# Optimization experiments

Measured on AMD Instinct MI355X. Metric: run time of the kernel, lower is better.

## Reference

```python
import jax, jax.numpy as jnp
import numpy as np

N = 4096
STEPS = 32


def setup_inputs() -> dict:
    key = jax.random.key(0)
    k0, k1, k2, k3 = jax.random.split(key, 4)
    x = jax.random.normal(k0, (N, 2), dtype=jnp.float32) * 0.02
    raw_S = jax.random.normal(k1, (N, N), dtype=jnp.float32) * 0.1
    raw_phase = jax.random.normal(k2, (N, N), dtype=jnp.float32) * 0.1
    # raw_r initialized at logit(p_r0=0.2) in the original module
    init_logit = float(np.log(0.2 / 0.8))
    raw_r = jnp.full((N, N), init_logit, dtype=jnp.float32)
    mask = (jax.random.uniform(k3, (N, N)) < 0.1).astype(jnp.float32)
    A_mask = jnp.maximum(mask, jnp.eye(N, dtype=jnp.float32))
    G_gate = jnp.ones((N, N), dtype=jnp.float32)
    omega = jnp.float32(0.1)
    return {"x": x, "raw_S": raw_S, "raw_phase": raw_phase, "raw_r": raw_r,
            "A_mask": A_mask, "G_gate": G_gate, "omega": omega, "steps": STEPS}


def reference(x, raw_S, raw_phase, raw_r, A_mask, G_gate, omega, steps):
    # Effective amplitude adjacency (beta=0, no do-interventions): same at every step
    S = jnp.tanh(raw_S)
    r = jax.nn.sigmoid(raw_r)
    Aamp = A_mask * G_gate * S * r  # [N, N]

    def step(xc, t):
        theta = raw_phase + omega * t          # [N, N] time-varying phase
        c = jnp.cos(theta)
        s = jnp.sin(theta)
        xr = xc[:, 0]  # [N]
        xi = xc[:, 1]  # [N]
        out_r = (Aamp * c) @ xr - (Aamp * s) @ xi
        out_i = (Aamp * s) @ xr + (Aamp * c) @ xi
        x_next = jnp.stack([jnp.tanh(out_r), jnp.tanh(out_i)], axis=-1)  # [N, 2]
        return x_next, x_next

    ts = jnp.arange(steps, dtype=x.dtype)
    _, traj = jax.lax.scan(step, x, ts)
    return jnp.concatenate([x[None], traj], axis=0)  # [steps+1, N, 2]
```

## Files before the change

kernel.cpp:

```cpp
#include <hip/hip_runtime.h>
#include <cstdint>
#include <cstddef>

#define N 4096
#define STEPS 32
#define PADW 640

__device__ __forceinline__ float bf16lo_to_f(uint32_t u) {
    return __uint_as_float(u << 16);
}
__device__ __forceinline__ float bf16hi_to_f(uint32_t u) {
    return __uint_as_float(u & 0xFFFF0000u);
}
__device__ __forceinline__ uint32_t f_to_bf16bits(float f) {
    uint32_t u = __float_as_uint(f);
    return (u + 0x7FFFu + ((u >> 16) & 1u)) >> 16;
}
__device__ __forceinline__ float fast_tanh(float x) {
    float e = __expf(2.0f * x);
    return (e - 1.0f) * __builtin_amdgcn_rcpf(e + 1.0f);
}
__device__ __forceinline__ float fast_sigmoid(float x) {
    return __builtin_amdgcn_rcpf(1.0f + __expf(-x));
}


__global__ __launch_bounds__(256) void fill_sparse_kernel(
    const float* __restrict__ raw_S,
    const float* __restrict__ raw_phase,
    const float* __restrict__ raw_r,
    const float* __restrict__ A_mask,
    const float* __restrict__ G_gate,
    uint16_t* __restrict__ col16,
    uint32_t* __restrict__ val32)
{
    const int wave = threadIdx.x >> 6;
    const int lane = threadIdx.x & 63;
    const int row  = blockIdx.x * 4 + wave;
    const size_t rbase = (size_t)row * N;
    const size_t pbase = (size_t)row * PADW;

    int base = 0;
    size_t off0 = rbase + lane * 4;
    float4 m4 = *(const float4*)(A_mask + off0);
    float4 g4 = *(const float4*)(G_gate + off0);
    float4 s4 = *(const float4*)(raw_S + off0);
    float4 r4 = *(const float4*)(raw_r + off0);
    float4 p4 = *(const float4*)(raw_phase + off0);

#pragma unroll 2
    for (int j = 0; j < N / 256; j++) {
        float mv[4] = {m4.x, m4.y, m4.z, m4.w};
        float gv[4] = {g4.x, g4.y, g4.z, g4.w};
        float sv[4] = {s4.x, s4.y, s4.z, s4.w};
        float rv[4] = {r4.x, r4.y, r4.z, r4.w};
        float pv[4] = {p4.x, p4.y, p4.z, p4.w};
        if (j < N / 256 - 1) {
            size_t off = rbase + (j + 1) * 256 + lane * 4;
            m4 = *(const float4*)(A_mask + off);
            g4 = *(const float4*)(G_gate + off);
            s4 = *(const float4*)(raw_S + off);
            r4 = *(const float4*)(raw_r + off);
            p4 = *(const float4*)(raw_phase + off);
        }

        uint32_t pk[4];
        bool pr[4];
#pragma unroll
        for (int k = 0; k < 4; k++) {
            pr[k] = (mv[k] != 0.0f);
            float S  = fast_tanh(sv[k]);
            float rr = fast_sigmoid(rv[k]);
            float amp = mv[k] * gv[k] * S * rr;
            uint32_t pc = f_to_bf16bits(amp * __cosf(pv[k]));
            uint32_t ps = f_to_bf16bits(amp * __sinf(pv[k]));
            pk[k] = (ps << 16) | pc;
        }
#pragma unroll
        for (int k = 0; k < 4; k++) {
            unsigned long long bal = __ballot(pr[k]);
            if (pr[k]) {
                int idx = base + __popcll(bal & ((1ull << lane) - 1ull));
                if (idx < PADW) {
                    col16[pbase + idx] = (uint16_t)(j * 256 + lane * 4 + k);
                    val32[pbase + idx] = pk[k];
                }
            }
            base += (int)__popcll(bal);
        }
    }
    if (base > PADW) base = PADW;
    for (int i = base + lane; i < PADW; i += 64) {
        col16[pbase + i] = 0;
        val32[pbase + i] = 0;
    }
}

__global__ __launch_bounds__(256) void step_sparse_kernel(
    const uint16_t* __restrict__ col16,
    const uint32_t* __restrict__ val32,
    const float* __restrict__ x_in,
    float* __restrict__ x_out,
    const float* __restrict__ omega_ptr,
    int t)
{
    __shared__ float xs[2 * N];
    const int tid = threadIdx.x;
    {
        const float4* src = (const float4*)x_in;
        float4* dst = (float4*)xs;
#pragma unroll
        for (int i = 0; i < 8; i++)
            dst[tid + 256 * i] = src[tid + 256 * i];
    }
    __syncthreads();

    const int wave = tid >> 6;
    const int lane = tid & 63;
    const int row = blockIdx.x * 4 + wave;

    const uint32_t* colp = (const uint32_t*)(col16 + (size_t)row * PADW);
    const uint2*    valp = (const uint2*)(val32 + (size_t)row * PADW);

    float are = 0.0f, aim = 0.0f;
#pragma unroll
    for (int j = 0; j < PADW / 128; j++) {
        uint32_t cc = colp[j * 64 + lane];
        uint2    vv = valp[j * 64 + lane];
        int c0 = (int)(cc & 0xFFFFu), c1 = (int)(cc >> 16);
        float2 x0 = *(const float2*)(xs + 2 * c0);
        float2 x1 = *(const float2*)(xs + 2 * c1);
        float pc0 = bf16lo_to_f(vv.x), ps0 = bf16hi_to_f(vv.x);
        float pc1 = bf16lo_to_f(vv.y), ps1 = bf16hi_to_f(vv.y);
        are = fmaf(pc0, x0.x, are); are = fmaf(-ps0, x0.y, are);
        aim = fmaf(ps0, x0.x, aim); aim = fmaf(pc0, x0.y, aim);
        are = fmaf(pc1, x1.x, are); are = fmaf(-ps1, x1.y, are);
        aim = fmaf(ps1, x1.x, aim); aim = fmaf(pc1, x1.y, aim);
    }
#pragma unroll
    for (int off = 32; off; off >>= 1) {
        are += __shfl_down(are, off);
        aim += __shfl_down(aim, off);
    }
    if (lane == 0) {
        float theta = omega_ptr[0] * (float)t;
        float st, ct;
        __sincosf(theta, &st, &ct);
        float ore = ct * are - st * aim;
        float oim = st * are + ct * aim;
        *(float2*)(x_out + 2 * row) =
            make_float2(fast_tanh(ore), fast_tanh(oim));
    }
}


__global__ __launch_bounds__(256) void precompute_kernel(
    const float* __restrict__ raw_phase,
    const float* __restrict__ raw_r,
    const float* __restrict__ A_mask,
    const float* __restrict__ G_gate,
    const float* raw_S_in,
    float* dst)
{
    int idx = (blockIdx.x * 256 + threadIdx.x) * 4;
    float4 s4 = *(const float4*)(raw_S_in + idx);
    float4 p4 = *(const float4*)(raw_phase + idx);
    float4 r4 = *(const float4*)(raw_r + idx);
    float4 m4 = *(const float4*)(A_mask + idx);
    float4 g4 = *(const float4*)(G_gate + idx);
    float sv[4] = {s4.x, s4.y, s4.z, s4.w};
    float pv[4] = {p4.x, p4.y, p4.z, p4.w};
    float rv[4] = {r4.x, r4.y, r4.z, r4.w};
    float mv[4] = {m4.x, m4.y, m4.z, m4.w};
    float gv[4] = {g4.x, g4.y, g4.z, g4.w};
    float ov[4];
#pragma unroll
    for (int k = 0; k < 4; k++) {
        float S = fast_tanh(sv[k]);
        float r = fast_sigmoid(rv[k]);
        float amp = mv[k] * gv[k] * S * r;
        uint32_t pc = f_to_bf16bits(amp * __cosf(pv[k]));
        uint32_t ps = f_to_bf16bits(amp * __sinf(pv[k]));
        ov[k] = __uint_as_float((ps << 16) | pc);
    }
    *(float4*)(dst + idx) = make_float4(ov[0], ov[1], ov[2], ov[3]);
}

__global__ __launch_bounds__(512, 8) void step_kernel(
    const float* __restrict__ Mpacked_f,
    const float* __restrict__ x_in,
    float* __restrict__ x_out,
    const float* __restrict__ omega_ptr,
    int t)
{
    const int tid  = threadIdx.x;
    const int wave = tid >> 6;
    const int lane = tid & 63;
    const int row0 = blockIdx.x * 4;
    const uint32_t* M = (const uint32_t*)Mpacked_f;
    const int cbase = (wave << 9) + (lane << 2);
    float xr[8], xi[8];
#pragma unroll
    for (int s = 0; s < 2; s++) {
        int j = cbase + (s << 8);
        float4 a = *(const float4*)(x_in + 2 * j);
        float4 b = *(const float4*)(x_in + 2 * j + 4);
        xr[4*s+0]=a.x; xi[4*s+0]=a.y; xr[4*s+1]=a.z; xi[4*s+1]=a.w;
        xr[4*s+2]=b.x; xi[4*s+2]=b.y; xr[4*s+3]=b.z; xi[4*s+3]=b.w;
    }
    __shared__ float part[8][4][2];
#pragma unroll
    for (int r = 0; r < 4; r++) {
        const uint32_t* Mrow = M + (size_t)(row0 + r) * N + cbase;
        float are = 0.0f, aim = 0.0f;
#pragma unroll
        for (int s = 0; s < 2; s++) {
            uint4 m = *(const uint4*)(Mrow + (s << 8));
            uint32_t mm[4] = {m.x, m.y, m.z, m.w};
#pragma unroll
            for (int k = 0; k < 4; k++) {
                float pc = bf16lo_to_f(mm[k]);
                float ps = bf16hi_to_f(mm[k]);
                float xre = xr[4*s+k], xim = xi[4*s+k];
                are = fmaf(pc, xre, are); are = fmaf(-ps, xim, are);
                aim = fmaf(ps, xre, aim); aim = fmaf(pc, xim, aim);
            }
        }
#pragma unroll
        for (int off = 32; off; off >>= 1) {
            are += __shfl_down(are, off);
            aim += __shfl_down(aim, off);
        }
        if (lane == 0) { part[wave][r][0] = are; part[wave][r][1] = aim; }
    }
    __syncthreads();
    if (tid < 4) {
        float U = 0.0f, V = 0.0f;
#pragma unroll
        for (int w = 0; w < 8; w++) { U += part[w][tid][0]; V += part[w][tid][1]; }
        float theta = omega_ptr[0] * (float)t;
        float stv, ctv;
        __sincosf(theta, &stv, &ctv);
        float ore = ctv * U - stv * V;
        float oim = stv * U + ctv * V;
        int row = row0 + tid;
        x_out[2*row+0] = fast_tanh(ore);
        x_out[2*row+1] = fast_tanh(oim);
    }
}


extern "C" void kernel_launch(void* const* d_in, const int* in_sizes, int n_in,
                              void* d_out, int out_size, void* d_ws, size_t ws_size,
                              hipStream_t stream) {
    const float* x         = (const float*)d_in[0];
    float*       raw_S     = (float*)d_in[1];
    const float* raw_phase = (const float*)d_in[2];
    const float* raw_r     = (const float*)d_in[3];
    const float* A_mask    = (const float*)d_in[4];
    const float* G_gate    = (const float*)d_in[5];
    const float* omega     = (const float*)d_in[6];
    float* out = (float*)d_out;

    hipMemcpyAsync(out, x, (size_t)N * 2 * sizeof(float),
                   hipMemcpyDeviceToDevice, stream);

    const size_t colBytes = (size_t)N * PADW * sizeof(uint16_t);
    const size_t valBytes = (size_t)N * PADW * sizeof(uint32_t);
    if (ws_size >= colBytes + valBytes) {
        uint16_t* col16 = (uint16_t*)d_ws;
        uint32_t* val32 = (uint32_t*)((char*)d_ws + colBytes);

        fill_sparse_kernel<<<dim3(N / 4), dim3(256), 0, stream>>>(
            raw_S, raw_phase, raw_r, A_mask, G_gate, col16, val32);

        for (int t = 0; t < STEPS; t++) {
            step_sparse_kernel<<<dim3(N / 4), dim3(256), 0, stream>>>(
                col16, val32,
                out + (size_t)t * N * 2,
                out + (size_t)(t + 1) * N * 2,
                omega, t);
        }
    } else {
        float* packed = raw_S;
        precompute_kernel<<<dim3(N * (N / 1024)), dim3(256), 0, stream>>>(
            raw_phase, raw_r, A_mask, G_gate, raw_S, packed);
        for (int t = 0; t < STEPS; t++) {
            step_kernel<<<dim3(N / 4), dim3(512), 0, stream>>>(
                packed,
                out + (size_t)t * N * 2,
                out + (size_t)(t + 1) * N * 2,
                omega, t);
        }
    }
}
```

Before: 453.5 us.

## Fuse all steps into persistent kernel with grid barrier and register-resident sparse matrix

Replaces the 32 per-step launches with a single persistent kernel of 256 blocks of 1024 threads. Each wave keeps its row's sparse values and column indices in registers across all steps, and blocks synchronise through a global atomic-counter barrier. The fill kernel is also split so each row is handled by two waves over half-rows, with a fixed per-half capacity of 320 nonzeros. This removes launch overhead and repeated sparse-matrix reloads, but it relies on all 256 blocks being co-resident. The half-row cap can also drop entries if nonzeros are unevenly split between the two halves.

```diff
diff --git a/kernel.cpp b/kernel.cpp
--- a/kernel.cpp
+++ b/kernel.cpp
@@ -5,6 +5,8 @@
 #define N 4096
 #define STEPS 32
 #define PADW 640
+#define HALFW 320
+#define PGRID 256
 
 __device__ __forceinline__ float bf16lo_to_f(uint32_t u) {
     return __uint_as_float(u << 16);
@@ -23,7 +25,6 @@
 __device__ __forceinline__ float fast_sigmoid(float x) {
     return __builtin_amdgcn_rcpf(1.0f + __expf(-x));
 }
-
 
 __global__ __launch_bounds__(256) void fill_sparse_kernel(
     const float* __restrict__ raw_S,
@@ -34,11 +35,13 @@
     uint16_t* __restrict__ col16,
     uint32_t* __restrict__ val32)
 {
-    const int wave = threadIdx.x >> 6;
-    const int lane = threadIdx.x & 63;
-    const int row  = blockIdx.x * 4 + wave;
-    const size_t rbase = (size_t)row * N;
-    const size_t pbase = (size_t)row * PADW;
+    const int wave   = threadIdx.x >> 6;
+    const int lane   = threadIdx.x & 63;
+    const int halfid = blockIdx.x * 4 + wave;
+    const int row    = halfid >> 1;
+    const int h      = halfid & 1;
+    const size_t rbase = (size_t)row * N + (size_t)h * (N / 2);
+    const size_t pbase = (size_t)row * PADW + (size_t)h * HALFW;
 
     int base = 0;
     size_t off0 = rbase + lane * 4;
@@ -49,13 +52,13 @@
     float4 p4 = *(const float4*)(raw_phase + off0);
 
 #pragma unroll 2
-    for (int j = 0; j < N / 256; j++) {
+    for (int j = 0; j < (N / 2) / 256; j++) {
         float mv[4] = {m4.x, m4.y, m4.z, m4.w};
         float gv[4] = {g4.x, g4.y, g4.z, g4.w};
         float sv[4] = {s4.x, s4.y, s4.z, s4.w};
         float rv[4] = {r4.x, r4.y, r4.z, r4.w};
         float pv[4] = {p4.x, p4.y, p4.z, p4.w};
-        if (j < N / 256 - 1) {
+        if (j < (N / 2) / 256 - 1) {
             size_t off = rbase + (j + 1) * 256 + lane * 4;
             m4 = *(const float4*)(A_mask + off);
             g4 = *(const float4*)(G_gate + off);
@@ -81,75 +84,104 @@
             unsigned long long bal = __ballot(pr[k]);
             if (pr[k]) {
                 int idx = base + __popcll(bal & ((1ull << lane) - 1ull));
-                if (idx < PADW) {
-                    col16[pbase + idx] = (uint16_t)(j * 256 + lane * 4 + k);
+                if (idx < HALFW) {
+                    col16[pbase + idx] =
+                        (uint16_t)(h * (N / 2) + j * 256 + lane * 4 + k);
                     val32[pbase + idx] = pk[k];
                 }
             }
             base += (int)__popcll(bal);
         }
     }
-    if (base > PADW) base = PADW;
-    for (int i = base + lane; i < PADW; i += 64) {
+    if (base > HALFW) base = HALFW;
+    for (int i = base + lane; i < HALFW; i += 64) {
         col16[pbase + i] = 0;
         val32[pbase + i] = 0;
     }
 }
 
-__global__ __launch_bounds__(256) void step_sparse_kernel(
+__global__ __launch_bounds__(1024, 4) void persistent_steps_kernel(
     const uint16_t* __restrict__ col16,
     const uint32_t* __restrict__ val32,
-    const float* __restrict__ x_in,
-    float* __restrict__ x_out,
+    float* out,
     const float* __restrict__ omega_ptr,
-    int t)
+    unsigned int* barrier_cnt)
 {
     __shared__ float xs[2 * N];
-    const int tid = threadIdx.x;
-    {
-        const float4* src = (const float4*)x_in;
-        float4* dst = (float4*)xs;
-#pragma unroll
-        for (int i = 0; i < 8; i++)
-            dst[tid + 256 * i] = src[tid + 256 * i];
-    }
-    __syncthreads();
-
+    const int tid  = threadIdx.x;
     const int wave = tid >> 6;
     const int lane = tid & 63;
-    const int row = blockIdx.x * 4 + wave;
-
-    const uint32_t* colp = (const uint32_t*)(col16 + (size_t)row * PADW);
-    const uint2*    valp = (const uint2*)(val32 + (size_t)row * PADW);
-
-    float are = 0.0f, aim = 0.0f;
-#pragma unroll
-    for (int j = 0; j < PADW / 128; j++) {
-        uint32_t cc = colp[j * 64 + lane];
-        uint2    vv = valp[j * 64 + lane];
-        int c0 = (int)(cc & 0xFFFFu), c1 = (int)(cc >> 16);
-        float2 x0 = *(const float2*)(xs + 2 * c0);
-        float2 x1 = *(const float2*)(xs + 2 * c1);
-        float pc0 = bf16lo_to_f(vv.x), ps0 = bf16hi_to_f(vv.x);
-        float pc1 = bf16lo_to_f(vv.y), ps1 = bf16hi_to_f(vv.y);
-        are = fmaf(pc0, x0.x, are); are = fmaf(-ps0, x0.y, are);
-        aim = fmaf(ps0, x0.x, aim); aim = fmaf(pc0, x0.y, aim);
-        are = fmaf(pc1, x1.x, are); are = fmaf(-ps1, x1.y, are);
-        aim = fmaf(ps1, x1.x, aim); aim = fmaf(pc1, x1.y, aim);
-    }
-#pragma unroll
-    for (int off = 32; off; off >>= 1) {
-        are += __shfl_down(are, off);
-        aim += __shfl_down(aim, off);
-    }
-    if (lane == 0) {
-        float theta = omega_ptr[0] * (float)t;
-        float st, ct;
-        __sincosf(theta, &st, &ct);
-        float ore = ct * are - st * aim;
-        float oim = st * are + ct * aim;
-        *(float2*)(x_out + 2 * row) =
-            make_float2(fast_tanh(ore), fast_tanh(oim));
+    const int row  = blockIdx.x * 16 + wave;
+
+    uint32_t cidx[10];
+    float pcv[10], psv[10];
+    {
+        const size_t base = (size_t)row * PADW;
+#pragma unroll
+        for (int s = 0; s < 10; s++) {
+            uint16_t c = col16[base + s * 64 + lane];
+            uint32_t v = val32[base + s * 64 + lane];
+            cidx[s] = 2u * (uint32_t)c;
+            pcv[s] = bf16lo_to_f(v);
+            psv[s] = bf16hi_to_f(v);
+        }
+    }
+    const float om = omega_ptr[0];
+
+    {
+        const float4* src = (const float4*)out;
+        float4* dst = (float4*)xs;
+        dst[tid]        = src[tid];
+        dst[tid + 1024] = src[tid + 1024];
+    }
+    __syncthreads();
+
+    for (int t = 0; t < STEPS; t++) {
+        float are = 0.0f, aim = 0.0f;
+#pragma unroll
+        for (int s = 0; s < 10; s++) {
+            float2 xv = *(const float2*)(xs + cidx[s]);
+            are = fmaf(pcv[s], xv.x, are);
+            are = fmaf(-psv[s], xv.y, are);
+            aim = fmaf(psv[s], xv.x, aim);
+            aim = fmaf(pcv[s], xv.y, aim);
+        }
+#pragma unroll
+        for (int off = 32; off; off >>= 1) {
+            are += __shfl_down(are, off);
+            aim += __shfl_down(aim, off);
+        }
+        if (lane == 0) {
+            float theta = om * (float)t;
+            float st, ct;
+            __sincosf(theta, &st, &ct);
+            float ore = ct * are - st * aim;
+            float oim = st * are + ct * aim;
+            *(float2*)(out + (size_t)(t + 1) * 2 * N + 2 * row) =
+                make_float2(fast_tanh(ore), fast_tanh(oim));
+        }
+
+        __syncthreads();
+        if (tid == 0) {
+            __hip_atomic_fetch_add(barrier_cnt, 1u, __ATOMIC_RELEASE,
+                                   __HIP_MEMORY_SCOPE_AGENT);
+            const unsigned int target = (unsigned int)PGRID * (t + 1);
+            long guard = 0;
+            while (__hip_atomic_load(barrier_cnt, __ATOMIC_ACQUIRE,
+                                     __HIP_MEMORY_SCOPE_AGENT) < target) {
+                __builtin_amdgcn_s_sleep(2);
+                if (++guard > 20000000L) break;
+            }
+        }
+        __syncthreads();
+
+        {
+            const float4* src = (const float4*)(out + (size_t)(t + 1) * 2 * N);
+            float4* dst = (float4*)xs;
+            dst[tid]        = src[tid];
+            dst[tid + 1024] = src[tid + 1024];
+        }
+        __syncthreads();
     }
 }
 
@@ -267,20 +299,18 @@
 
     const size_t colBytes = (size_t)N * PADW * sizeof(uint16_t);
     const size_t valBytes = (size_t)N * PADW * sizeof(uint32_t);
-    if (ws_size >= colBytes + valBytes) {
-        uint16_t* col16 = (uint16_t*)d_ws;
-        uint32_t* val32 = (uint32_t*)((char*)d_ws + colBytes);
-
-        fill_sparse_kernel<<<dim3(N / 4), dim3(256), 0, stream>>>(
+    if (ws_size >= 128 + colBytes + valBytes) {
+        unsigned int* cnt = (unsigned int*)d_ws;
+        uint16_t* col16 = (uint16_t*)((char*)d_ws + 128);
+        uint32_t* val32 = (uint32_t*)((char*)d_ws + 128 + colBytes);
+
+        hipMemsetAsync(cnt, 0, 128, stream);
+
+        fill_sparse_kernel<<<dim3(N / 2), dim3(256), 0, stream>>>(
             raw_S, raw_phase, raw_r, A_mask, G_gate, col16, val32);
 
-        for (int t = 0; t < STEPS; t++) {
-            step_sparse_kernel<<<dim3(N / 4), dim3(256), 0, stream>>>(
-                col16, val32,
-                out + (size_t)t * N * 2,
-                out + (size_t)(t + 1) * N * 2,
-                omega, t);
-        }
+        persistent_steps_kernel<<<dim3(PGRID), dim3(1024), 0, stream>>>(
+            col16, val32, out, omega, cnt);
     } else {
         float* packed = raw_S;
         precompute_kernel<<<dim3(N * (N / 1024)), dim3(256), 0, stream>>>(
```

After: 685.5 us. 51.2% more time.

## Split sparse fill into quarter-row waves and widen step blocks to 16 rows

Applied to the files above, without the earlier changes.

The fill kernel now gives each wave a quarter of a row (1024 columns) with a fixed 160-slot segment of the padded ELL row. It loads all 4 chunks up front instead of serially prefetching 16 chunks, which gives 4x more waves and more memory-level parallelism on the expensive 5-matrix read. The step kernel uses 1024-thread blocks covering 16 rows, so each block stages the x vector into shared memory for 4x more rows. Risk: per-quarter capacity of 160 entries can overflow where a row's nonzeros are unevenly spread, whereas before the whole row shared 640 slots. The padded zero entries also change layout within each row.

```diff
diff --git a/kernel.cpp b/kernel.cpp
--- a/kernel.cpp
+++ b/kernel.cpp
@@ -5,6 +5,7 @@
 #define N 4096
 #define STEPS 32
 #define PADW 640
+#define QW 160
 
 __device__ __forceinline__ float bf16lo_to_f(uint32_t u) {
     return __uint_as_float(u << 16);
@@ -23,7 +24,6 @@
 __device__ __forceinline__ float fast_sigmoid(float x) {
     return __builtin_amdgcn_rcpf(1.0f + __expf(-x));
 }
-
 
 __global__ __launch_bounds__(256) void fill_sparse_kernel(
     const float* __restrict__ raw_S,
@@ -36,33 +36,31 @@
 {
     const int wave = threadIdx.x >> 6;
     const int lane = threadIdx.x & 63;
-    const int row  = blockIdx.x * 4 + wave;
-    const size_t rbase = (size_t)row * N;
-    const size_t pbase = (size_t)row * PADW;
+    const int qid  = blockIdx.x * 4 + wave;
+    const int row  = qid >> 2;
+    const int q    = qid & 3;
+    const size_t rbase = (size_t)row * N + (size_t)q * (N / 4);
+    const size_t pbase = (size_t)row * PADW + (size_t)q * QW;
+
+    float4 mb[4], gb[4], sb[4], rb[4], pb[4];
+#pragma unroll
+    for (int c = 0; c < 4; c++) {
+        size_t off = rbase + (size_t)c * 256 + (size_t)lane * 4;
+        mb[c] = *(const float4*)(A_mask + off);
+        gb[c] = *(const float4*)(G_gate + off);
+        sb[c] = *(const float4*)(raw_S + off);
+        rb[c] = *(const float4*)(raw_r + off);
+        pb[c] = *(const float4*)(raw_phase + off);
+    }
 
     int base = 0;
-    size_t off0 = rbase + lane * 4;
-    float4 m4 = *(const float4*)(A_mask + off0);
-    float4 g4 = *(const float4*)(G_gate + off0);
-    float4 s4 = *(const float4*)(raw_S + off0);
-    float4 r4 = *(const float4*)(raw_r + off0);
-    float4 p4 = *(const float4*)(raw_phase + off0);
-
-#pragma unroll 2
-    for (int j = 0; j < N / 256; j++) {
-        float mv[4] = {m4.x, m4.y, m4.z, m4.w};
-        float gv[4] = {g4.x, g4.y, g4.z, g4.w};
-        float sv[4] = {s4.x, s4.y, s4.z, s4.w};
-        float rv[4] = {r4.x, r4.y, r4.z, r4.w};
-        float pv[4] = {p4.x, p4.y, p4.z, p4.w};
-        if (j < N / 256 - 1) {
-            size_t off = rbase + (j + 1) * 256 + lane * 4;
-            m4 = *(const float4*)(A_mask + off);
-            g4 = *(const float4*)(G_gate + off);
-            s4 = *(const float4*)(raw_S + off);
-            r4 = *(const float4*)(raw_r + off);
-            p4 = *(const float4*)(raw_phase + off);
-        }
+#pragma unroll
+    for (int c = 0; c < 4; c++) {
+        float mv[4] = {mb[c].x, mb[c].y, mb[c].z, mb[c].w};
+        float gv[4] = {gb[c].x, gb[c].y, gb[c].z, gb[c].w};
+        float sv[4] = {sb[c].x, sb[c].y, sb[c].z, sb[c].w};
+        float rv[4] = {rb[c].x, rb[c].y, rb[c].z, rb[c].w};
+        float pv[4] = {pb[c].x, pb[c].y, pb[c].z, pb[c].w};
 
         uint32_t pk[4];
         bool pr[4];
@@ -81,22 +79,23 @@
             unsigned long long bal = __ballot(pr[k]);
             if (pr[k]) {
                 int idx = base + __popcll(bal & ((1ull << lane) - 1ull));
-                if (idx < PADW) {
-                    col16[pbase + idx] = (uint16_t)(j * 256 + lane * 4 + k);
+                if (idx < QW) {
+                    col16[pbase + idx] =
+                        (uint16_t)(q * (N / 4) + c * 256 + lane * 4 + k);
                     val32[pbase + idx] = pk[k];
                 }
             }
             base += (int)__popcll(bal);
         }
     }
-    if (base > PADW) base = PADW;
-    for (int i = base + lane; i < PADW; i += 64) {
+    if (base > QW) base = QW;
+    for (int i = base + lane; i < QW; i += 64) {
         col16[pbase + i] = 0;
         val32[pbase + i] = 0;
     }
 }
 
-__global__ __launch_bounds__(256) void step_sparse_kernel(
+__global__ __launch_bounds__(1024) void step_sparse_kernel(
     const uint16_t* __restrict__ col16,
     const uint32_t* __restrict__ val32,
     const float* __restrict__ x_in,
@@ -109,15 +108,14 @@
     {
         const float4* src = (const float4*)x_in;
         float4* dst = (float4*)xs;
-#pragma unroll
-        for (int i = 0; i < 8; i++)
-            dst[tid + 256 * i] = src[tid + 256 * i];
+        dst[tid]        = src[tid];
+        dst[tid + 1024] = src[tid + 1024];
     }
     __syncthreads();
 
     const int wave = tid >> 6;
     const int lane = tid & 63;
-    const int row = blockIdx.x * 4 + wave;
+    const int row = blockIdx.x * 16 + wave;
 
     const uint32_t* colp = (const uint32_t*)(col16 + (size_t)row * PADW);
     const uint2*    valp = (const uint2*)(val32 + (size_t)row * PADW);
@@ -271,11 +269,11 @@
         uint16_t* col16 = (uint16_t*)d_ws;
         uint32_t* val32 = (uint32_t*)((char*)d_ws + colBytes);
 
-        fill_sparse_kernel<<<dim3(N / 4), dim3(256), 0, stream>>>(
+        fill_sparse_kernel<<<dim3(N), dim3(256), 0, stream>>>(
             raw_S, raw_phase, raw_r, A_mask, G_gate, col16, val32);
 
         for (int t = 0; t < STEPS; t++) {
-            step_sparse_kernel<<<dim3(N / 4), dim3(256), 0, stream>>>(
+            step_sparse_kernel<<<dim3(N / 16), dim3(1024), 0, stream>>>(
                 col16, val32,
                 out + (size_t)t * N * 2,
                 out + (size_t)(t + 1) * N * 2,
```

New measurement: 425.3 us. 6.2% less time.
